# Optimization experiments

Measured on AMD Instinct MI355X. Metric: run time of the kernel, lower is better.

The kernel has to match this reference:

```python
import jax, jax.numpy as jnp
import numpy as np

# Module hyperparameters (from init_kwargs)
B = 8          # batch_size
NV = 8192      # num_template_vertices
NS = 4096      # num_fixed_samples
NPD = 64       # round(NS ** 0.5)
L_BOUND = 0.0
U_BOUND = 1.0
BD = (U_BOUND - L_BOUND) / (NPD - 1)   # min_sigma default
D_DIM = 2.0
C = (4.0 / (D_DIM + 2)) ** (1.0 / (D_DIM + 4)) * NV ** (-1.0 / (D_DIM + 4))
CF = (2.0 * np.pi) ** (-D_DIM / 2) / C ** D_DIM
CN = -1.0 / (2.0 * C ** 2)


def _make_grid():
    g = jnp.linspace(L_BOUND, U_BOUND, NPD, dtype=jnp.float32)
    gx, gy = jnp.meshgrid(g, g, indexing='ij')          # torch.meshgrid default 'ij'
    S = jnp.stack([gx, gy], axis=-1).reshape(NPD * NPD, 2)
    return jnp.broadcast_to(S[None], (B, NPD * NPD, 2))  # [B, npd^2, 2]


def setup_inputs() -> dict:
    key = jax.random.key(0)
    T = jax.random.uniform(key, (B, NV, 2), dtype=jnp.float32)  # UV in [0,1]
    S = _make_grid()
    return {"T": T, "S": S}


def reference(T, S):
    # sigma: per-batch bandwidth from vertex spread (torch std is unbiased, ddof=1)
    sigma = jnp.clip(jnp.std(T, axis=1, ddof=1).mean(axis=-1), BD)  # [B]
    # batched squared-L2 cdist: D[b,i,j] = ||S[b,i] - T[b,j]||^2  -> [B, npd^2, nV]
    s2 = jnp.sum(S * S, axis=-1)[:, :, None]
    t2 = jnp.sum(T * T, axis=-1)[:, None, :]
    cross = jnp.einsum('bik,bjk->bij', S, T)
    D = s2 + t2 - 2.0 * cross
    # Gaussian kernel density estimate at each grid point, mean over vertices
    E = jnp.exp(CN * D / (sigma[:, None, None] ** 2))
    K_H = CF * sigma[:, None] ** (-D_DIM) * E.mean(axis=-1)    # [B, npd^2]
    # normalize to a histogram
    return K_H / jnp.clip(K_H.sum(axis=1, keepdims=True), 1e-05)
```

## Files before the change

### kernel.cpp

```cpp
#include <hip/hip_runtime.h>
#include <math.h>

#define BATCH 8
#define NVERT 8192
#define NPD   64
#define NCELL 4096
#define SPLITS 64
#define JPB   (NVERT / SPLITS)
#define G     16
#define ROUNDS (JPB / G)

#ifndef M_PI
#define M_PI 3.14159265358979323846
#endif

#define TOTPART_OFF  0
#define PARAMS_OFF   1024
#define PARTIALS_OFF 4096

static __device__ __forceinline__ float fast_exp2(float x) {
#if __has_builtin(__builtin_amdgcn_exp2f)
    return __builtin_amdgcn_exp2f(x);
#else
    return exp2f(x);
#endif
}

__global__ __launch_bounds__(256) void kde_kernel(const float* __restrict__ T,
                                                  float* __restrict__ params,
                                                  float* __restrict__ totpart,
                                                  float* __restrict__ partials) {
    const int b   = blockIdx.x >> 6;
    const int sp  = blockIdx.x & (SPLITS - 1);
    const int j0  = sp * JPB;
    const int tid = threadIdx.x;
    const int w    = tid >> 6;
    const int lane = tid & 63;

    __shared__ float  smem_es[2 * G * 128];
    __shared__ float  gB[NCELL];
    __shared__ float2 tj[JPB];
    __shared__ float  red[4][4];
    __shared__ float  bcast[2];
    float* gA = smem_es;

    const float4* T4 = reinterpret_cast<const float4*>(T + (size_t)b * NVERT * 2);
    float sx = 0.f, sx2 = 0.f, sy = 0.f, sy2 = 0.f;
    for (int q = tid; q < NVERT / 2; q += 256) {
        float4 v = T4[q];
        sx += v.x + v.z;
        sy += v.y + v.w;
        sx2 += v.x * v.x + v.z * v.z;
        sy2 += v.y * v.y + v.w * v.w;
        int local = 2 * q - j0;
        if ((unsigned)local < (unsigned)JPB)
            *reinterpret_cast<float4*>(&tj[local]) = v;
    }
    for (int off = 32; off; off >>= 1) {
        sx  += __shfl_down(sx,  off);  sx2 += __shfl_down(sx2, off);
        sy  += __shfl_down(sy,  off);  sy2 += __shfl_down(sy2, off);
    }
    if (lane == 0) { red[w][0] = sx; red[w][1] = sx2; red[w][2] = sy; red[w][3] = sy2; }
    __syncthreads();
    if (tid == 0) {
        double tsx = 0, tsx2 = 0, tsy = 0, tsy2 = 0;
        for (int i = 0; i < 4; ++i) {
            tsx += red[i][0]; tsx2 += red[i][1]; tsy += red[i][2]; tsy2 += red[i][3];
        }
        const double N = (double)NVERT;
        double varx = (tsx2 - tsx * tsx / N) / (N - 1.0);
        double vary = (tsy2 - tsy * tsy / N) / (N - 1.0);
        double sigma = 0.5 * (sqrt(varx) + sqrt(vary));
        const double BD = 1.0 / 63.0;
        if (sigma < BD) sigma = BD;
        const double C2 = pow(2.0, -13.0 / 3.0);
        double s2 = sigma * sigma;
        bcast[0] = (float)(-0.5 / C2 / (s2 * 0.69314718055994530942));
        bcast[1] = (float)(1.0 / (2.0 * M_PI * C2) / (s2 * N));
        if (sp == 0) params[b] = bcast[1];
    }
    __syncthreads();
    const float kexp2 = bcast[0];

    const int   c     = tid & 127;
    const bool  isX   = (c < 64);
    const float xc    = (float)(c & 63) * (1.0f / 63.0f);
    const int   gbase = tid >> 7;

#define STAGE(JG, BUF)                                                    \
    {                                                                     \
        _Pragma("unroll")                                                 \
        for (int r_ = 0; r_ < 8; ++r_) {                                  \
            int g = r_ * 2 + gbase;                                       \
            float2 t2 = tj[(JG) + g];                                     \
            float tv = isX ? t2.x : t2.y;                                 \
            float d = xc - tv;                                            \
            smem_es[((BUF) * G + g) * 128 + c] = fast_exp2(kexp2 * d * d);\
        }                                                                 \
    }

    const int tx = lane >> 3;
    const int ty = lane & 7;
    float acc[8][8];
#pragma unroll
    for (int i = 0; i < 8; ++i)
#pragma unroll
        for (int j = 0; j < 8; ++j) acc[i][j] = 0.0f;

    STAGE(0, 0);
    for (int r = 0; r < ROUNDS; ++r) {
        __syncthreads();
        if (r + 1 < ROUNDS) STAGE((r + 1) * G, (r + 1) & 1);
        const float* E = &smem_es[(r & 1) * G * 128];
#pragma unroll
        for (int v = 0; v < 4; ++v) {
            const float* row = &E[((w << 2) + v) * 128];
            float4 ex0 = *reinterpret_cast<const float4*>(&row[tx * 8]);
            float4 ex1 = *reinterpret_cast<const float4*>(&row[tx * 8 + 4]);
            float4 ey0 = *reinterpret_cast<const float4*>(&row[64 + ty * 8]);
            float4 ey1 = *reinterpret_cast<const float4*>(&row[64 + ty * 8 + 4]);
            float ex[8] = {ex0.x, ex0.y, ex0.z, ex0.w, ex1.x, ex1.y, ex1.z, ex1.w};
            float ey[8] = {ey0.x, ey0.y, ey0.z, ey0.w, ey1.x, ey1.y, ey1.z, ey1.w};
#pragma unroll
            for (int i = 0; i < 8; ++i)
#pragma unroll
                for (int j = 0; j < 8; ++j)
                    acc[i][j] = fmaf(ex[i], ey[j], acc[i][j]);
        }
    }

    __syncthreads();
    float* gw = (w & 2) ? gB : gA;
    if (!(w & 1)) {
#pragma unroll
        for (int i = 0; i < 8; ++i) {
            int base = (tx * 8 + i) * 64 + ty * 8;
            *reinterpret_cast<float4*>(&gw[base]) =
                make_float4(acc[i][0], acc[i][1], acc[i][2], acc[i][3]);
            *reinterpret_cast<float4*>(&gw[base + 4]) =
                make_float4(acc[i][4], acc[i][5], acc[i][6], acc[i][7]);
        }
    }
    __syncthreads();
    if (w & 1) {
#pragma unroll
        for (int i = 0; i < 8; ++i) {
            int base = (tx * 8 + i) * 64 + ty * 8;
            float4 a = *reinterpret_cast<const float4*>(&gw[base]);
            float4 h = *reinterpret_cast<const float4*>(&gw[base + 4]);
            a.x += acc[i][0]; a.y += acc[i][1]; a.z += acc[i][2]; a.w += acc[i][3];
            h.x += acc[i][4]; h.y += acc[i][5]; h.z += acc[i][6]; h.w += acc[i][7];
            *reinterpret_cast<float4*>(&gw[base])     = a;
            *reinterpret_cast<float4*>(&gw[base + 4]) = h;
        }
    }
    __syncthreads();
    float* dst = partials + (size_t)blockIdx.x * NCELL;
    float tsum = 0.f;
#pragma unroll
    for (int q = 0; q < 4; ++q) {
        int f = q * 256 + tid;
        float4 a = reinterpret_cast<const float4*>(gA)[f];
        float4 bb = reinterpret_cast<const float4*>(gB)[f];
        float4 r = make_float4(a.x + bb.x, a.y + bb.y, a.z + bb.z, a.w + bb.w);
        reinterpret_cast<float4*>(dst)[f] = r;
        tsum += (r.x + r.y) + (r.z + r.w);
    }
    for (int off = 32; off; off >>= 1) tsum += __shfl_down(tsum, off);
    if (lane == 0) red[w][0] = tsum;
    __syncthreads();
    if (tid == 0)
        totpart[blockIdx.x] = (red[0][0] + red[1][0]) + (red[2][0] + red[3][0]);
}

__global__ __launch_bounds__(128) void finish_kernel(const float* __restrict__ partials,
                                                     const float* __restrict__ totpart,
                                                     const float* __restrict__ params,
                                                     float* __restrict__ out) {
    const int b     = blockIdx.x >> 5;
    const int strip = blockIdx.x & 31;
    const int cell  = strip * 128 + threadIdx.x;
    const float* p  = partials + (size_t)b * SPLITS * NCELL + cell;

    float s[8] = {0.f, 0.f, 0.f, 0.f, 0.f, 0.f, 0.f, 0.f};
#pragma unroll
    for (int k8 = 0; k8 < 8; ++k8)
#pragma unroll
        for (int j = 0; j < 8; ++j)
            s[j] += p[(size_t)(k8 * 8 + j) * NCELL];
    float sum = ((s[0] + s[1]) + (s[2] + s[3])) + ((s[4] + s[5]) + (s[6] + s[7]));

    __shared__ float tot_s;
    if (threadIdx.x < 64) {
        float v = totpart[b * SPLITS + threadIdx.x];
        for (int off = 32; off; off >>= 1) v += __shfl_down(v, off);
        if (threadIdx.x == 0) tot_s = v;
    }
    __syncthreads();

    const float scale = params[b];
    const float denom = fmaxf(tot_s * scale, 1e-5f);
    out[b * NCELL + cell] = (sum * scale) / denom;
}

extern "C" void kernel_launch(void* const* d_in, const int* in_sizes, int n_in,
                              void* d_out, int out_size, void* d_ws, size_t ws_size,
                              hipStream_t stream) {
    const float* T = (const float*)d_in[0];

    float* ws       = (float*)d_ws;
    float* totpart  = ws + TOTPART_OFF;
    float* params   = ws + PARAMS_OFF;
    float* partials = ws + PARTIALS_OFF;

    kde_kernel<<<BATCH * SPLITS, 256, 0, stream>>>(T, params, totpart, partials);
    finish_kernel<<<BATCH * 32, 128, 0, stream>>>(partials, totpart, params,
                                                  (float*)d_out);
}
```

Baseline: 76.67 us.

## Compute separable KDE outer-product sums with bf16 MFMA instead of FP32 FMAs

Replaces the per-thread 8x8 FP32 outer-product accumulation with MFMA 16x16x32 bf16 instructions. The per-axis Gaussian factors are packed to bf16 in transposed LDS tiles, and each wave owns a 16-row slab of the 64x64 grid. This removes the cross-wave LDS reduction and its extra syncs, and results are written directly from the accumulators. It lowers precision of the exponential factors to bf16, which may raise error in the normalized histogram.

Result: faster. 69.47 us (-9.4%).

```diff
diff --git a/kernel.cpp b/kernel.cpp
--- a/kernel.cpp
+++ b/kernel.cpp
@@ -7,8 +7,8 @@
 #define NCELL 4096
 #define SPLITS 64
 #define JPB   (NVERT / SPLITS)
-#define G     16
-#define ROUNDS (JPB / G)
+#define KR    32
+#define ROUNDS (JPB / KR)
 
 #ifndef M_PI
 #define M_PI 3.14159265358979323846
@@ -18,12 +18,22 @@
 #define PARAMS_OFF   1024
 #define PARTIALS_OFF 4096
 
+typedef __attribute__((ext_vector_type(8))) short  bf16x8;
+typedef __attribute__((ext_vector_type(4))) float  f32x4;
+
 static __device__ __forceinline__ float fast_exp2(float x) {
 #if __has_builtin(__builtin_amdgcn_exp2f)
     return __builtin_amdgcn_exp2f(x);
 #else
     return exp2f(x);
 #endif
+}
+
+static __device__ __forceinline__ unsigned int pack_bf16(float a, float b) {
+    unsigned int ua = __float_as_uint(a), ub = __float_as_uint(b);
+    ua += 0x7fffu + ((ua >> 16) & 1u);
+    ub += 0x7fffu + ((ub >> 16) & 1u);
+    return (ua >> 16) | (ub & 0xffff0000u);
 }
 
 __global__ __launch_bounds__(256) void kde_kernel(const float* __restrict__ T,
@@ -37,12 +47,11 @@
     const int w    = tid >> 6;
     const int lane = tid & 63;
 
-    __shared__ float  smem_es[2 * G * 128];
-    __shared__ float  gB[NCELL];
+    __shared__ __align__(16) unsigned short exT[2][64][40];
+    __shared__ __align__(16) unsigned short eyT[2][64][40];
     __shared__ float2 tj[JPB];
     __shared__ float  red[4][4];
     __shared__ float  bcast[2];
-    float* gA = smem_es;
 
     const float4* T4 = reinterpret_cast<const float4*>(T + (size_t)b * NVERT * 2);
     float sx = 0.f, sx2 = 0.f, sy = 0.f, sy2 = 0.f;
@@ -82,89 +91,56 @@
     __syncthreads();
     const float kexp2 = bcast[0];
 
-    const int   c     = tid & 127;
-    const bool  isX   = (c < 64);
-    const float xc    = (float)(c & 63) * (1.0f / 63.0f);
-    const int   gbase = tid >> 7;
+    const float xg   = (float)lane * (1.0f / 63.0f);
+    const int   jh   = (w >> 1) << 4;
+    const bool  isY  = (w & 1);
 
-#define STAGE(JG, BUF)                                                    \
-    {                                                                     \
-        _Pragma("unroll")                                                 \
-        for (int r_ = 0; r_ < 8; ++r_) {                                  \
-            int g = r_ * 2 + gbase;                                       \
-            float2 t2 = tj[(JG) + g];                                     \
-            float tv = isX ? t2.x : t2.y;                                 \
-            float d = xc - tv;                                            \
-            smem_es[((BUF) * G + g) * 128 + c] = fast_exp2(kexp2 * d * d);\
-        }                                                                 \
+#define STAGE(R, BUF)                                                       \
+    {                                                                       \
+        unsigned short (*dstT)[40] = isY ? eyT[BUF] : exT[BUF];             \
+        _Pragma("unroll")                                                   \
+        for (int jp = 0; jp < 8; ++jp) {                                    \
+            int jl = jh + jp * 2;                                           \
+            float4 tt = *reinterpret_cast<const float4*>(&tj[(R) * KR + jl]);\
+            float tv0 = isY ? tt.y : tt.x;                                  \
+            float tv1 = isY ? tt.w : tt.z;                                  \
+            float d0 = xg - tv0, d1 = xg - tv1;                             \
+            float e0 = fast_exp2(kexp2 * d0 * d0);                          \
+            float e1 = fast_exp2(kexp2 * d1 * d1);                          \
+            *reinterpret_cast<unsigned int*>(&dstT[lane][jl]) =             \
+                pack_bf16(e0, e1);                                          \
+        }                                                                   \
     }
 
-    const int tx = lane >> 3;
-    const int ty = lane & 7;
-    float acc[8][8];
+    const int col16 = lane & 15;
+    const int kq    = lane >> 4;
+    f32x4 acc[4];
 #pragma unroll
-    for (int i = 0; i < 8; ++i)
-#pragma unroll
-        for (int j = 0; j < 8; ++j) acc[i][j] = 0.0f;
+    for (int ni = 0; ni < 4; ++ni) acc[ni] = (f32x4){0.f, 0.f, 0.f, 0.f};
 
     STAGE(0, 0);
     for (int r = 0; r < ROUNDS; ++r) {
         __syncthreads();
-        if (r + 1 < ROUNDS) STAGE((r + 1) * G, (r + 1) & 1);
-        const float* E = &smem_es[(r & 1) * G * 128];
+        if (r + 1 < ROUNDS) STAGE(r + 1, (r + 1) & 1);
+        const int buf = r & 1;
+        bf16x8 af = *reinterpret_cast<const bf16x8*>(&exT[buf][(w << 4) + col16][kq << 3]);
 #pragma unroll
-        for (int v = 0; v < 4; ++v) {
-            const float* row = &E[((w << 2) + v) * 128];
-            float4 ex0 = *reinterpret_cast<const float4*>(&row[tx * 8]);
-            float4 ex1 = *reinterpret_cast<const float4*>(&row[tx * 8 + 4]);
-            float4 ey0 = *reinterpret_cast<const float4*>(&row[64 + ty * 8]);
-            float4 ey1 = *reinterpret_cast<const float4*>(&row[64 + ty * 8 + 4]);
-            float ex[8] = {ex0.x, ex0.y, ex0.z, ex0.w, ex1.x, ex1.y, ex1.z, ex1.w};
-            float ey[8] = {ey0.x, ey0.y, ey0.z, ey0.w, ey1.x, ey1.y, ey1.z, ey1.w};
-#pragma unroll
-            for (int i = 0; i < 8; ++i)
-#pragma unroll
-                for (int j = 0; j < 8; ++j)
-                    acc[i][j] = fmaf(ex[i], ey[j], acc[i][j]);
+        for (int ni = 0; ni < 4; ++ni) {
+            bf16x8 bfr = *reinterpret_cast<const bf16x8*>(&eyT[buf][(ni << 4) + col16][kq << 3]);
+            acc[ni] = __builtin_amdgcn_mfma_f32_16x16x32_bf16(af, bfr, acc[ni], 0, 0, 0);
         }
     }
 
-    __syncthreads();
-    float* gw = (w & 2) ? gB : gA;
-    if (!(w & 1)) {
-#pragma unroll
-        for (int i = 0; i < 8; ++i) {
-            int base = (tx * 8 + i) * 64 + ty * 8;
-            *reinterpret_cast<float4*>(&gw[base]) =
-                make_float4(acc[i][0], acc[i][1], acc[i][2], acc[i][3]);
-            *reinterpret_cast<float4*>(&gw[base + 4]) =
-                make_float4(acc[i][4], acc[i][5], acc[i][6], acc[i][7]);
-        }
-    }
-    __syncthreads();
-    if (w & 1) {
-#pragma unroll
-        for (int i = 0; i < 8; ++i) {
-            int base = (tx * 8 + i) * 64 + ty * 8;
-            float4 a = *reinterpret_cast<const float4*>(&gw[base]);
-            float4 h = *reinterpret_cast<const float4*>(&gw[base + 4]);
-            a.x += acc[i][0]; a.y += acc[i][1]; a.z += acc[i][2]; a.w += acc[i][3];
-            h.x += acc[i][4]; h.y += acc[i][5]; h.z += acc[i][6]; h.w += acc[i][7];
-            *reinterpret_cast<float4*>(&gw[base])     = a;
-            *reinterpret_cast<float4*>(&gw[base + 4]) = h;
-        }
-    }
-    __syncthreads();
     float* dst = partials + (size_t)blockIdx.x * NCELL;
     float tsum = 0.f;
+    const int rowbase = (w << 4) + (kq << 2);
 #pragma unroll
-    for (int q = 0; q < 4; ++q) {
-        int f = q * 256 + tid;
-        float4 a = reinterpret_cast<const float4*>(gA)[f];
-        float4 bb = reinterpret_cast<const float4*>(gB)[f];
-        float4 r = make_float4(a.x + bb.x, a.y + bb.y, a.z + bb.z, a.w + bb.w);
-        reinterpret_cast<float4*>(dst)[f] = r;
-        tsum += (r.x + r.y) + (r.z + r.w);
+    for (int ni = 0; ni < 4; ++ni) {
+#pragma unroll
+        for (int r = 0; r < 4; ++r) {
+            dst[(rowbase + r) * 64 + (ni << 4) + col16] = acc[ni][r];
+            tsum += acc[ni][r];
+        }
     }
     for (int off = 32; off; off >>= 1) tsum += __shfl_down(tsum, off);
     if (lane == 0) red[w][0] = tsum;
```
